# Performance work log

Measured on AMD Instinct MI355X. Metric: run time of the kernel, lower is better.

The kernel has to match this reference:

```python
import jax, jax.numpy as jnp
import numpy as np

B = 1024
E = 200          # entity_dim (== relation_dim)
R = 200          # relation_dim
NE = 50000       # num_entities
NR = 400         # num_relations
OC = 32          # out_channels
FW = 9           # filt_w (filt_h = 1)
WP = E - FW + 1  # conv output width = 192
FC_IN = OC * WP  # 6144
EPS = 1e-5


def setup_inputs() -> dict:
    key = jax.random.key(0)
    ks = jax.random.split(key, 20)
    s = lambda n: 1.0 / np.sqrt(n)
    inp = {
        "e_s": jax.random.randint(ks[0], (B,), 0, NE, dtype=jnp.int32),
        "q_s": jax.random.randint(ks[1], (B,), 0, NR, dtype=jnp.int32),
        "e_c": jax.random.randint(ks[2], (B,), 0, NE, dtype=jnp.int32),
        "entity_emb": jax.random.normal(ks[3], (NE, E), jnp.float32) * 0.1,
        "relation_emb": jax.random.normal(ks[4], (NR, R), jnp.float32) * 0.1,
        "W1_w": jax.random.normal(ks[5], (E + R, R), jnp.float32) * s(E + R),
        "W1_b": jnp.zeros((R,), jnp.float32),
        "fc1_w": jax.random.normal(ks[6], (R, OC * FW), jnp.float32) * s(R),
        "fc1_b": jnp.zeros((OC * FW,), jnp.float32),
        "fc_w": jax.random.normal(ks[7], (FC_IN, E), jnp.float32) * s(FC_IN),
        "fc_b": jnp.zeros((E,), jnp.float32),
        "bn0_g": jnp.ones((1,), jnp.float32),
        "bn0_b": jnp.zeros((1,), jnp.float32),
        "bn0_m": jnp.zeros((1,), jnp.float32),
        "bn0_v": jnp.ones((1,), jnp.float32),
        "bn1_g": jnp.ones((OC,), jnp.float32),
        "bn1_b": jnp.zeros((OC,), jnp.float32),
        "bn1_m": jnp.zeros((OC,), jnp.float32),
        "bn1_v": jnp.ones((OC,), jnp.float32),
        "bn2_g": jnp.ones((E,), jnp.float32),
        "bn2_b": jnp.zeros((E,), jnp.float32),
        "bn2_m": jnp.zeros((E,), jnp.float32),
        "bn2_v": jnp.ones((E,), jnp.float32),
        "bias_b": jnp.zeros((NE,), jnp.float32),
    }
    return inp


def reference(e_s, q_s, e_c, entity_emb, relation_emb, W1_w, W1_b,
              fc1_w, fc1_b, fc_w, fc_b,
              bn0_g, bn0_b, bn0_m, bn0_v,
              bn1_g, bn1_b, bn1_m, bn1_v,
              bn2_g, bn2_b, bn2_m, bn2_v, bias_b):
    es = entity_emb[e_s]                      # [B,E]
    ec = entity_emb[e_c]                      # [B,E]
    r = relation_emb[q_s]                     # [B,R]
    # W1: Linear(E+R -> R); here R == E so e1 has width E
    e1 = jnp.concatenate([es, ec], -1) @ W1_w + W1_b          # [B,E]
    # bn0: single channel, inference mode
    x = (e1 - bn0_m) * (bn0_g / jnp.sqrt(bn0_v + EPS)) + bn0_b  # [B,E]
    # per-sample dynamic filters from fc1(r)
    k = (r @ fc1_w + fc1_b).reshape(B, OC, FW)                # [B,OC,FW]
    # grouped conv (groups=B) == per-sample 1D sliding dot products
    patches = jnp.stack([x[:, w:w + WP] for w in range(FW)], axis=-1)  # [B,WP,FW]
    conv = jnp.einsum('bpw,bow->bop', patches, k)             # [B,OC,WP]
    # bn1 over the OC channel, inference mode
    conv = (conv - bn1_m[:, None]) * (bn1_g / jnp.sqrt(bn1_v + EPS))[:, None] + bn1_b[:, None]
    flat = conv.reshape(B, FC_IN)                             # [B, OC*WP]
    h = flat @ fc_w + fc_b                                    # [B,E]
    h = (h - bn2_m) * (bn2_g / jnp.sqrt(bn2_v + EPS)) + bn2_b
    h = jax.nn.relu(h)
    logits = h @ entity_emb.T + bias_b                        # [B,NE]
    return jax.nn.sigmoid(logits)
```

## Files before the change

kernel.cpp:

```cpp
#include <hip/hip_runtime.h>

#define B_   1024
#define E_   200
#define NE_  50000
#define OC_  32
#define FW_  9
#define WP_  192
#define FCIN 6144
#define CATK 400
#define KDIM 288

typedef __attribute__((ext_vector_type(8))) short short8;
typedef __attribute__((ext_vector_type(4))) float floatx4;
typedef __attribute__((ext_vector_type(4))) unsigned short ushort4v;

static __device__ __forceinline__ float bf2f(unsigned short u) {
  return __uint_as_float(((unsigned)u) << 16);
}
static __device__ __forceinline__ unsigned short f2bf(float f) {
  unsigned u = __float_as_uint(f);
  u += 0x7FFFu + ((u >> 16) & 1u);
  return (unsigned short)(u >> 16);
}

__global__ __launch_bounds__(256) void k_cvt(
    const float* __restrict__ in, unsigned short* __restrict__ out, int n4) {
  int i = blockIdx.x * 256 + threadIdx.x;
  if (i >= n4) return;
  float4 v = ((const float4*)in)[i];
  ushort4v o = {f2bf(v.x), f2bf(v.y), f2bf(v.z), f2bf(v.w)};
  ((ushort4v*)out)[i] = o;
}

__global__ __launch_bounds__(256) void k_gather(
    const int* __restrict__ e_s, const int* __restrict__ q_s, const int* __restrict__ e_c,
    const float* __restrict__ ent, const float* __restrict__ rel,
    unsigned short* __restrict__ cat, unsigned short* __restrict__ rbuf) {
  int idx = blockIdx.x * 256 + threadIdx.x;
  if (idx < B_ * CATK) {
    int s = idx / CATK, i = idx - s * CATK;
    int row = (i < E_) ? e_s[s] : e_c[s];
    int col = (i < E_) ? i : i - E_;
    cat[idx] = f2bf(ent[row * E_ + col]);
  } else {
    int j = idx - B_ * CATK;
    if (j < B_ * E_) {
      int s = j / E_, i = j - s * E_;
      rbuf[j] = f2bf(rel[q_s[s] * E_ + i]);
    }
  }
}

__global__ __launch_bounds__(256) void k_transpose_lds(
    const float* __restrict__ in, unsigned short* __restrict__ out,
    int N, int Npad, int K) {
  __shared__ unsigned short lds[64][65];
  int n0 = blockIdx.x * 64, k0 = blockIdx.y * 64;
  int tx = threadIdx.x & 63, ty = threadIdx.x >> 6;
#pragma unroll
  for (int kk = 0; kk < 16; kk++) {
    int k = k0 + ty + 4 * kk;
    int n = n0 + tx;
    unsigned short v = 0;
    if (k < K && n < N) v = f2bf(in[(long)k * N + n]);
    lds[ty + 4 * kk][tx] = v;
  }
  __syncthreads();
#pragma unroll
  for (int kk = 0; kk < 16; kk++) {
    int k = k0 + tx;
    int n = n0 + ty + 4 * kk;
    if (n < Npad && k < K) out[(long)n * K + k] = lds[tx][ty + 4 * kk];
  }
}

template<int NK, int RQ>
static __device__ __forceinline__ floatx4 gemm_64x16(
    const unsigned short* __restrict__ A, int lda,
    const unsigned short* __restrict__ Bt, int ldb, int m0, int n0) {
  int lane = threadIdx.x & 63;
  int wv   = threadIdx.x >> 6;
  int l16  = lane & 15, quad = lane >> 4;
  const unsigned short* ap = A  + (long)(m0 + 16 * wv + l16) * lda + quad * 8;
  const unsigned short* bp = Bt + (long)(n0 + l16) * ldb + quad * 8;
  floatx4 acc = {0.f, 0.f, 0.f, 0.f};
#pragma unroll 4
  for (int ks = 0; ks < NK; ks++) {
    short8 a = *(const short8*)(ap + ks * 32);
    short8 b = *(const short8*)(bp + ks * 32);
    acc = __builtin_amdgcn_mfma_f32_16x16x32_bf16(a, b, acc, 0, 0, 0);
  }
  if (RQ > 0) {
    short8 z = {0,0,0,0,0,0,0,0};
    short8 a = (quad < RQ) ? *(const short8*)(ap + NK * 32) : z;
    short8 b = (quad < RQ) ? *(const short8*)(bp + NK * 32) : z;
    acc = __builtin_amdgcn_mfma_f32_16x16x32_bf16(a, b, acc, 0, 0, 0);
  }
  return acc;
}

__global__ __launch_bounds__(256) void k_gemm_e1(
    const unsigned short* __restrict__ cat, const unsigned short* __restrict__ W1T,
    const float* __restrict__ W1b,
    const float* __restrict__ g0, const float* __restrict__ b0,
    const float* __restrict__ m0p, const float* __restrict__ v0,
    unsigned short* __restrict__ xbuf) {
  int m0 = blockIdx.x * 64, n0 = blockIdx.y * 16;
  floatx4 acc = gemm_64x16<12, 2>(cat, CATK, W1T, CATK, m0, n0);
  int lane = threadIdx.x & 63, wv = threadIdx.x >> 6;
  int l16 = lane & 15, quad = lane >> 4;
  int j = n0 + l16;
  if (j < E_) {
    float s0  = g0[0] * rsqrtf(v0[0] + 1e-5f);
    float off = (W1b[j] - m0p[0]) * s0 + b0[0];
    int rbase = m0 + 16 * wv + quad * 4;
#pragma unroll
    for (int i = 0; i < 4; i++)
      xbuf[(rbase + i) * E_ + j] = f2bf(acc[i] * s0 + off);
  }
}

__global__ __launch_bounds__(256) void k_gemm_k(
    const unsigned short* __restrict__ rbuf, const unsigned short* __restrict__ fc1T,
    const float* __restrict__ fc1b,
    const float* __restrict__ g1, const float* __restrict__ v1,
    unsigned short* __restrict__ kbuf) {
  int m0 = blockIdx.x * 64, n0 = blockIdx.y * 16;
  floatx4 acc = gemm_64x16<6, 1>(rbuf, E_, fc1T, E_, m0, n0);
  int lane = threadIdx.x & 63, wv = threadIdx.x >> 6;
  int l16 = lane & 15, quad = lane >> 4;
  int c = n0 + l16;
  int o = c / FW_;
  float s1 = g1[o] * rsqrtf(v1[o] + 1e-5f);
  float fb = fc1b[c];
  int rbase = m0 + 16 * wv + quad * 4;
#pragma unroll
  for (int i = 0; i < 4; i++)
    kbuf[(rbase + i) * KDIM + c] = f2bf((acc[i] + fb) * s1);
}

__global__ __launch_bounds__(256) void k_conv(
    const unsigned short* __restrict__ xbuf, const unsigned short* __restrict__ kbuf,
    const float* __restrict__ g1, const float* __restrict__ b1,
    const float* __restrict__ m1, const float* __restrict__ v1,
    unsigned short* __restrict__ flat) {
  __shared__ float xs[E_];
  __shared__ float ks[KDIM];
  __shared__ float beta[OC_];
  int b = blockIdx.x, tid = threadIdx.x;
  if (tid < E_)  xs[tid] = bf2f(xbuf[b * E_ + tid]);
  for (int i = tid; i < KDIM; i += 256) ks[i] = bf2f(kbuf[b * KDIM + i]);
  if (tid < OC_) {
    float s = g1[tid] * rsqrtf(v1[tid] + 1e-5f);
    beta[tid] = b1[tid] - m1[tid] * s;
  }
  __syncthreads();
#pragma unroll
  for (int u = 0; u < FCIN / 256; u++) {
    int t = u * 256 + tid;
    int o = t / WP_, p = t - o * WP_;
    float acc = beta[o];
#pragma unroll
    for (int w = 0; w < FW_; w++) acc += xs[p + w] * ks[o * FW_ + w];
    flat[b * FCIN + t] = f2bf(acc);
  }
}

__global__ __launch_bounds__(256) void k_gemm_fc(
    const unsigned short* __restrict__ flat, const unsigned short* __restrict__ fcwT,
    float* __restrict__ partial) {
  int m0 = blockIdx.x * 64, n0 = blockIdx.y * 16, kc = blockIdx.z;
  int lane = threadIdx.x & 63, wv = threadIdx.x >> 6;
  int l16 = lane & 15, quad = lane >> 4;
  const unsigned short* ap = flat + (long)(m0 + 16 * wv + l16) * FCIN + kc * 768 + quad * 8;
  const unsigned short* bp = fcwT + (long)(n0 + l16) * FCIN + kc * 768 + quad * 8;
  floatx4 acc = {0.f, 0.f, 0.f, 0.f};
#pragma unroll 4
  for (int ks = 0; ks < 24; ks++) {
    short8 a = *(const short8*)(ap + ks * 32);
    short8 b = *(const short8*)(bp + ks * 32);
    acc = __builtin_amdgcn_mfma_f32_16x16x32_bf16(a, b, acc, 0, 0, 0);
  }
  int j = n0 + l16;
  int rbase = m0 + 16 * wv + quad * 4;
#pragma unroll
  for (int i = 0; i < 4; i++)
    partial[((long)kc * B_ + rbase + i) * 208 + j] = acc[i];
}

__global__ __launch_bounds__(256) void k_fc_epi(
    const float* __restrict__ partial, const float* __restrict__ fcb,
    const float* __restrict__ g2, const float* __restrict__ b2,
    const float* __restrict__ m2, const float* __restrict__ v2,
    unsigned short* __restrict__ hbuf) {
  int idx = blockIdx.x * 256 + threadIdx.x;
  if (idx >= B_ * E_) return;
  int m = idx / E_, j = idx - m * E_;
  float s = 0.f;
#pragma unroll
  for (int kc = 0; kc < 8; kc++) s += partial[((long)kc * B_ + m) * 208 + j];
  float s2 = g2[j] * rsqrtf(v2[j] + 1e-5f);
  float h = (s + fcb[j] - m2[j]) * s2 + b2[j];
  hbuf[idx] = f2bf(fmaxf(h, 0.f));
}

__global__ __launch_bounds__(256) void k_gemm_out(
    const unsigned short* __restrict__ hbuf, const unsigned short* __restrict__ entb,
    const float* __restrict__ bias, float* __restrict__ out) {
  int g  = blockIdx.y * 8 + blockIdx.x;
  int gp = (g & 7) * 782 + (g >> 3);
  int m0 = (gp & 7) * 128;
  int n0 = (gp >> 3) * 64;
  int lane = threadIdx.x & 63, wv = threadIdx.x >> 6;
  int l16 = lane & 15, quad = lane >> 4;

  const unsigned short* ap0 = hbuf + (long)(m0 + 32 * wv + l16) * E_ + quad * 8;
  const unsigned short* ap1 = ap0 + 16 * E_;
  int nb = n0 + 4 * l16;
  bool ok = nb < NE_;
  const unsigned short* bp[4];
#pragma unroll
  for (int f = 0; f < 4; f++) {
    int n = nb + f;
    bp[f] = entb + (long)((n < NE_) ? n : 0) * E_ + quad * 8;
  }

  floatx4 acc[8];
#pragma unroll
  for (int i = 0; i < 8; i++) acc[i] = (floatx4){0.f, 0.f, 0.f, 0.f};

#pragma unroll 2
  for (int ks = 0; ks < 6; ks++) {
    short8 a0 = *(const short8*)(ap0 + ks * 32);
    short8 a1 = *(const short8*)(ap1 + ks * 32);
#pragma unroll
    for (int f = 0; f < 4; f++) {
      short8 b = *(const short8*)(bp[f] + ks * 32);
      acc[f]     = __builtin_amdgcn_mfma_f32_16x16x32_bf16(a0, b, acc[f], 0, 0, 0);
      acc[4 + f] = __builtin_amdgcn_mfma_f32_16x16x32_bf16(a1, b, acc[4 + f], 0, 0, 0);
    }
  }
  {
    short8 z = {0,0,0,0,0,0,0,0};
    short8 a0 = (quad == 0) ? *(const short8*)(ap0 + 192) : z;
    short8 a1 = (quad == 0) ? *(const short8*)(ap1 + 192) : z;
#pragma unroll
    for (int f = 0; f < 4; f++) {
      short8 b = (quad == 0) ? *(const short8*)(bp[f] + 192) : z;
      acc[f]     = __builtin_amdgcn_mfma_f32_16x16x32_bf16(a0, b, acc[f], 0, 0, 0);
      acc[4 + f] = __builtin_amdgcn_mfma_f32_16x16x32_bf16(a1, b, acc[4 + f], 0, 0, 0);
    }
  }

  if (!ok) return;
  float4 bi = *(const float4*)(bias + nb);
#pragma unroll
  for (int t = 0; t < 2; t++) {
#pragma unroll
    for (int i = 0; i < 4; i++) {
      int row = m0 + 32 * wv + 16 * t + quad * 4 + i;
      float4 v;
      v.x = 1.f / (1.f + __expf(-(acc[t * 4 + 0][i] + bi.x)));
      v.y = 1.f / (1.f + __expf(-(acc[t * 4 + 1][i] + bi.y)));
      v.z = 1.f / (1.f + __expf(-(acc[t * 4 + 2][i] + bi.z)));
      v.w = 1.f / (1.f + __expf(-(acc[t * 4 + 3][i] + bi.w)));
      *(float4*)(out + (long)row * NE_ + nb) = v;
    }
  }
}

extern "C" void kernel_launch(void* const* d_in, const int* in_sizes, int n_in,
                              void* d_out, int out_size, void* d_ws, size_t ws_size,
                              hipStream_t stream) {
  const int* e_s = (const int*)d_in[0];
  const int* q_s = (const int*)d_in[1];
  const int* e_c = (const int*)d_in[2];
  const float* ent  = (const float*)d_in[3];
  const float* rel  = (const float*)d_in[4];
  const float* W1w  = (const float*)d_in[5];
  const float* W1b  = (const float*)d_in[6];
  const float* fc1w = (const float*)d_in[7];
  const float* fc1b = (const float*)d_in[8];
  const float* fcw  = (const float*)d_in[9];
  const float* fcb  = (const float*)d_in[10];
  const float* g0 = (const float*)d_in[11];
  const float* b0 = (const float*)d_in[12];
  const float* m0 = (const float*)d_in[13];
  const float* v0 = (const float*)d_in[14];
  const float* g1 = (const float*)d_in[15];
  const float* b1 = (const float*)d_in[16];
  const float* m1 = (const float*)d_in[17];
  const float* v1 = (const float*)d_in[18];
  const float* g2 = (const float*)d_in[19];
  const float* b2 = (const float*)d_in[20];
  const float* m2 = (const float*)d_in[21];
  const float* v2 = (const float*)d_in[22];
  const float* bias = (const float*)d_in[23];
  float* out = (float*)d_out;

  char* w = (char*)d_ws;
  unsigned short* entb = (unsigned short*)(w + 0);
  unsigned short* cat  = (unsigned short*)(w + 20000256);
  unsigned short* rbuf = (unsigned short*)(w + 20819712);
  unsigned short* W1T  = (unsigned short*)(w + 21229568);
  unsigned short* fc1T = (unsigned short*)(w + 21396224);
  unsigned short* fcwT = (unsigned short*)(w + 21511680);
  unsigned short* xbuf = (unsigned short*)(w + 24067840);
  unsigned short* kbuf = (unsigned short*)(w + 24477696);
  unsigned short* flat = (unsigned short*)(w + 25067776);
  unsigned short* hbuf = (unsigned short*)(w + 37650944);
  float* partial       = (float*)(w + 38060800);

  k_cvt<<<dim3((NE_ * E_ / 4 + 255) / 256), dim3(256), 0, stream>>>(ent, entb, NE_ * E_ / 4);
  k_gather<<<dim3((B_ * CATK + B_ * E_) / 256), dim3(256), 0, stream>>>(
      e_s, q_s, e_c, ent, rel, cat, rbuf);
  k_transpose_lds<<<dim3(4, 7),  dim3(256), 0, stream>>>(W1w,  W1T,  200, 208, CATK);
  k_transpose_lds<<<dim3(5, 4),  dim3(256), 0, stream>>>(fc1w, fc1T, 288, 288, E_);
  k_transpose_lds<<<dim3(4, 96), dim3(256), 0, stream>>>(fcw,  fcwT, 200, 208, FCIN);

  k_gemm_e1<<<dim3(16, 13), dim3(256), 0, stream>>>(cat, W1T, W1b, g0, b0, m0, v0, xbuf);
  k_gemm_k<<<dim3(16, 18), dim3(256), 0, stream>>>(rbuf, fc1T, fc1b, g1, v1, kbuf);
  k_conv<<<dim3(B_), dim3(256), 0, stream>>>(xbuf, kbuf, g1, b1, m1, v1, flat);
  k_gemm_fc<<<dim3(16, 13, 8), dim3(256), 0, stream>>>(flat, fcwT, partial);
  k_fc_epi<<<dim3((B_ * E_ + 255) / 256), dim3(256), 0, stream>>>(
      partial, fcb, g2, b2, m2, v2, hbuf);
  k_gemm_out<<<dim3(8, 782), dim3(256), 0, stream>>>(hbuf, entb, bias, out);
}
```

Before: 447.3 us.

## Stage entity tile in LDS and enlarge output GEMM tile to 256x128

The final logits GEMM now uses 512-thread blocks that each cover a 256x128 output tile. The block first loads its 128-entity slice of the bf16 embedding table into shared memory, in a layout matching the MFMA operand pattern, so all eight waves reuse it instead of each re-reading B from global memory. Blocks are remapped so consecutive tiles within an XCD share entity columns, and each thread writes two float4s per row. The costs are more accumulator registers per thread (16 MFMA accumulators), a sync barrier with ~56KB of LDS per block, and a larger tail tile at the end of the entity dimension.

Result: faster. 426.0 us (-4.8%).

```diff
diff --git a/kernel.cpp b/kernel.cpp
--- a/kernel.cpp
+++ b/kernel.cpp
@@ -204,67 +204,85 @@
   hbuf[idx] = f2bf(fmaxf(h, 0.f));
 }
 
-__global__ __launch_bounds__(256) void k_gemm_out(
+__global__ __launch_bounds__(512, 4) void k_gemm_out(
     const unsigned short* __restrict__ hbuf, const unsigned short* __restrict__ entb,
     const float* __restrict__ bias, float* __restrict__ out) {
-  int g  = blockIdx.y * 8 + blockIdx.x;
-  int gp = (g & 7) * 782 + (g >> 3);
-  int m0 = (gp & 7) * 128;
-  int n0 = (gp >> 3) * 64;
-  int lane = threadIdx.x & 63, wv = threadIdx.x >> 6;
+  __shared__ __align__(16) unsigned short Blds[7 * 4 * 128 * 8];
+  int g = blockIdx.x;
+  int xcd = g & 7, local_ = g >> 3;
+  int T = (xcd < 4 ? xcd * 196 : 784 + (xcd - 4) * 195) + local_;
+  int mt = T & 3, nt = T >> 2;
+  int m0 = mt * 256, n0 = nt * 128;
+  int tid = threadIdx.x;
+
+#pragma unroll
+  for (int it = 0; it < 7; ++it) {
+    int idx = it * 512 + tid;
+    int ks = idx >> 9, qd = (idx >> 7) & 3, np = idx & 127;
+    int col = 8 * (np & 15) + (np >> 4);
+    int n = n0 + col;
+    int kb = ks * 32 + qd * 8;
+    short8 v = {0, 0, 0, 0, 0, 0, 0, 0};
+    if (kb < 200 && n < NE_) v = *(const short8*)(entb + (long)n * E_ + kb);
+    *(short8*)(Blds + idx * 8) = v;
+  }
+  __syncthreads();
+
+  int lane = tid & 63, wv = tid >> 6;
   int l16 = lane & 15, quad = lane >> 4;
-
-  const unsigned short* ap0 = hbuf + (long)(m0 + 32 * wv + l16) * E_ + quad * 8;
+  const unsigned short* ap0 = hbuf + (long)(m0 + wv * 32 + l16) * E_ + quad * 8;
   const unsigned short* ap1 = ap0 + 16 * E_;
-  int nb = n0 + 4 * l16;
-  bool ok = nb < NE_;
-  const unsigned short* bp[4];
-#pragma unroll
-  for (int f = 0; f < 4; f++) {
-    int n = nb + f;
-    bp[f] = entb + (long)((n < NE_) ? n : 0) * E_ + quad * 8;
-  }
-
-  floatx4 acc[8];
-#pragma unroll
-  for (int i = 0; i < 8; i++) acc[i] = (floatx4){0.f, 0.f, 0.f, 0.f};
-
-#pragma unroll 2
-  for (int ks = 0; ks < 6; ks++) {
+
+  floatx4 acc[16];
+#pragma unroll
+  for (int i = 0; i < 16; ++i) acc[i] = (floatx4){0.f, 0.f, 0.f, 0.f};
+
+#pragma unroll
+  for (int ks = 0; ks < 6; ++ks) {
     short8 a0 = *(const short8*)(ap0 + ks * 32);
     short8 a1 = *(const short8*)(ap1 + ks * 32);
-#pragma unroll
-    for (int f = 0; f < 4; f++) {
-      short8 b = *(const short8*)(bp[f] + ks * 32);
-      acc[f]     = __builtin_amdgcn_mfma_f32_16x16x32_bf16(a0, b, acc[f], 0, 0, 0);
-      acc[4 + f] = __builtin_amdgcn_mfma_f32_16x16x32_bf16(a1, b, acc[4 + f], 0, 0, 0);
+    const unsigned short* bb = Blds + (ks * 4 + quad) * 1024 + l16 * 8;
+#pragma unroll
+    for (int nf = 0; nf < 8; ++nf) {
+      short8 b = *(const short8*)(bb + nf * 128);
+      acc[nf]     = __builtin_amdgcn_mfma_f32_16x16x32_bf16(a0, b, acc[nf], 0, 0, 0);
+      acc[8 + nf] = __builtin_amdgcn_mfma_f32_16x16x32_bf16(a1, b, acc[8 + nf], 0, 0, 0);
     }
   }
   {
-    short8 z = {0,0,0,0,0,0,0,0};
+    short8 z = {0, 0, 0, 0, 0, 0, 0, 0};
     short8 a0 = (quad == 0) ? *(const short8*)(ap0 + 192) : z;
     short8 a1 = (quad == 0) ? *(const short8*)(ap1 + 192) : z;
-#pragma unroll
-    for (int f = 0; f < 4; f++) {
-      short8 b = (quad == 0) ? *(const short8*)(bp[f] + 192) : z;
-      acc[f]     = __builtin_amdgcn_mfma_f32_16x16x32_bf16(a0, b, acc[f], 0, 0, 0);
-      acc[4 + f] = __builtin_amdgcn_mfma_f32_16x16x32_bf16(a1, b, acc[4 + f], 0, 0, 0);
+    const unsigned short* bb = Blds + (24 + quad) * 1024 + l16 * 8;
+#pragma unroll
+    for (int nf = 0; nf < 8; ++nf) {
+      short8 b = *(const short8*)(bb + nf * 128);
+      acc[nf]     = __builtin_amdgcn_mfma_f32_16x16x32_bf16(a0, b, acc[nf], 0, 0, 0);
+      acc[8 + nf] = __builtin_amdgcn_mfma_f32_16x16x32_bf16(a1, b, acc[8 + nf], 0, 0, 0);
     }
   }
 
-  if (!ok) return;
-  float4 bi = *(const float4*)(bias + nb);
-#pragma unroll
-  for (int t = 0; t < 2; t++) {
-#pragma unroll
-    for (int i = 0; i < 4; i++) {
-      int row = m0 + 32 * wv + 16 * t + quad * 4 + i;
-      float4 v;
-      v.x = 1.f / (1.f + __expf(-(acc[t * 4 + 0][i] + bi.x)));
-      v.y = 1.f / (1.f + __expf(-(acc[t * 4 + 1][i] + bi.y)));
-      v.z = 1.f / (1.f + __expf(-(acc[t * 4 + 2][i] + bi.z)));
-      v.w = 1.f / (1.f + __expf(-(acc[t * 4 + 3][i] + bi.w)));
-      *(float4*)(out + (long)row * NE_ + nb) = v;
+  int nb = n0 + 8 * l16;
+  if (nb >= NE_) return;
+  float4 bi0 = *(const float4*)(bias + nb);
+  float4 bi1 = *(const float4*)(bias + nb + 4);
+#pragma unroll
+  for (int mf = 0; mf < 2; ++mf) {
+#pragma unroll
+    for (int i = 0; i < 4; ++i) {
+      int row = m0 + wv * 32 + mf * 16 + quad * 4 + i;
+      float4 v0, v1;
+      v0.x = 1.f / (1.f + __expf(-(acc[mf * 8 + 0][i] + bi0.x)));
+      v0.y = 1.f / (1.f + __expf(-(acc[mf * 8 + 1][i] + bi0.y)));
+      v0.z = 1.f / (1.f + __expf(-(acc[mf * 8 + 2][i] + bi0.z)));
+      v0.w = 1.f / (1.f + __expf(-(acc[mf * 8 + 3][i] + bi0.w)));
+      v1.x = 1.f / (1.f + __expf(-(acc[mf * 8 + 4][i] + bi1.x)));
+      v1.y = 1.f / (1.f + __expf(-(acc[mf * 8 + 5][i] + bi1.y)));
+      v1.z = 1.f / (1.f + __expf(-(acc[mf * 8 + 6][i] + bi1.z)));
+      v1.w = 1.f / (1.f + __expf(-(acc[mf * 8 + 7][i] + bi1.w)));
+      float* op = out + (long)row * NE_ + nb;
+      *(float4*)op = v0;
+      *(float4*)(op + 4) = v1;
     }
   }
 }
@@ -324,5 +342,5 @@
   k_gemm_fc<<<dim3(16, 13, 8), dim3(256), 0, stream>>>(flat, fcwT, partial);
   k_fc_epi<<<dim3((B_ * E_ + 255) / 256), dim3(256), 0, stream>>>(
       partial, fcb, g2, b2, m2, v2, hbuf);
-  k_gemm_out<<<dim3(8, 782), dim3(256), 0, stream>>>(hbuf, entb, bias, out);
-}
+  k_gemm_out<<<dim3(1564), dim3(512), 0, stream>>>(hbuf, entb, bias, out);
+}
```
